# Kernel optimization log

Hardware: AMD Instinct MI355X
Metric: run time of the kernel (lower is better)

The kernel has to match this reference:

```python
import jax, jax.numpy as jnp
import numpy as np

K = 3
PAD = 1
EPS = 1e-5


def _unfold(x, k, pad):
    # torch.nn.Unfold(k, dilation=1, padding=pad, stride=1): output [B, C*k*k, L]
    # with channel-major ordering (c, ki, kj) in the second dim.
    B, C, H, W = x.shape
    xp = jnp.pad(x, ((0, 0), (0, 0), (pad, pad), (pad, pad)))
    Ho = H + 2 * pad - k + 1
    Wo = W + 2 * pad - k + 1
    patches = jnp.stack(
        [xp[:, :, i:i + Ho, j:j + Wo] for i in range(k) for j in range(k)],
        axis=2,
    )  # [B, C, k*k, Ho, Wo]
    return patches.reshape(B, C * k * k, Ho * Wo)


def _conv1x1(x, w, b):
    return jnp.einsum('bchw,oc->bohw', x, w) + b[None, :, None, None]


def _bn(x, g, b):
    # training-mode BatchNorm2d: batch stats over (B,H,W), biased variance
    mu = x.mean(axis=(0, 2, 3), keepdims=True)
    var = x.var(axis=(0, 2, 3), keepdims=True)
    return (x - mu) * jax.lax.rsqrt(var + EPS) * g[None, :, None, None] + b[None, :, None, None]


def _tri(x, w, b, g, be):
    return jax.nn.relu(_bn(_conv1x1(x, w, b), g, be))


def reference(x, w1, b1, g1, be1, w2, b2, g2, be2, wf, bf, gf, bef):
    B, C, H, W = x.shape
    k2 = K * K
    c = k2 // 2
    tri1 = _tri(x, w1, b1, g1, be1)  # key map  [B,C,H,W] (m=1)
    tri2 = _tri(x, w2, b2, g2, be2)  # query map
    # NOTE: faithful to source: plain row-major reshape of [B, C*k2, L] -> [B, C, L, k2]
    ku = _unfold(tri1, K, PAD).reshape(B, C, -1, k2)
    qu = _unfold(tri2, K, PAD).reshape(B, C, -1, k2)
    logits = ku * qu[..., c:c + 1] + ku[..., c:c + 1] * qu
    dl_weight = jax.nn.softmax(logits, axis=-1)[:, None]  # [B,1,C,L,k2]
    xu = _unfold(x, K, PAD).reshape(B, 1, C, -1, k2)       # m=1 -> [B,1,C,L,k2]
    # NOTE: faithful to source: row-major reshape to [B, C, k2, L], sum over axis -2
    pre = (dl_weight * xu).reshape(B, C, k2, -1).sum(axis=-2).reshape(B, C, H, W)
    return jax.nn.relu(_bn(_conv1x1(pre, wf, bf), gf, bef))


def setup_inputs() -> dict:
    key = jax.random.key(0)
    B, C, O, H, W = 4, 256, 256, 64, 64
    ks = jax.random.split(key, 4)
    s = 1.0 / np.sqrt(C)
    return {
        'x': jax.random.normal(ks[0], (B, C, H, W), dtype=jnp.float32),
        'w1': jax.random.normal(ks[1], (C, C), dtype=jnp.float32) * s,
        'b1': jnp.zeros((C,), jnp.float32),
        'g1': jnp.ones((C,), jnp.float32),
        'be1': jnp.zeros((C,), jnp.float32),
        'w2': jax.random.normal(ks[2], (C, C), dtype=jnp.float32) * s,
        'b2': jnp.zeros((C,), jnp.float32),
        'g2': jnp.ones((C,), jnp.float32),
        'be2': jnp.zeros((C,), jnp.float32),
        'wf': jax.random.normal(ks[3], (O, C), dtype=jnp.float32) * s,
        'bf': jnp.zeros((O,), jnp.float32),
        'gf': jnp.ones((O,), jnp.float32),
        'bef': jnp.zeros((O,), jnp.float32),
    }
```

## Files before the change

kernel.cpp:

```cpp
#include <hip/hip_runtime.h>
#include <hip/hip_bf16.h>

#define L 4096
#define CCH 256
#define NB 4
#define KP 40
#define GOF 72
#define LOG2E 1.4426950408889634f

typedef __attribute__((ext_vector_type(8))) short short8;
typedef __attribute__((ext_vector_type(4))) float f32x4;
typedef unsigned short ushort_t;

__device__ __forceinline__ unsigned short f2bf(float f) {
    unsigned u = __builtin_bit_cast(unsigned, f);
    u += 0x7FFF + ((u >> 16) & 1);
    return (unsigned short)(u >> 16);
}
__device__ __forceinline__ unsigned pk_bf16(float a, float b) {
    __hip_bfloat162 h = __float22bfloat162_rn(make_float2(a, b));
    unsigned u;
    __builtin_memcpy(&u, &h, 4);
    return u;
}
__device__ __forceinline__ float bflo(unsigned w) {
    return __builtin_bit_cast(float, w << 16);
}
__device__ __forceinline__ float bfhi(unsigned w) {
    return __builtin_bit_cast(float, w & 0xFFFF0000u);
}
__device__ __forceinline__ float bfu(ushort_t h) {
    return __builtin_bit_cast(float, (unsigned)h << 16);
}

__global__ __launch_bounds__(256) void wcvt_k(
    const float* __restrict__ w1, const float* __restrict__ w2,
    const float* __restrict__ wf,
    ushort_t* __restrict__ wb1, ushort_t* __restrict__ wb2,
    ushort_t* __restrict__ wbf)
{
    const int mb = blockIdx.x >> 6;
    const int i  = (blockIdx.x & 63) * 256 + threadIdx.x;
    const float* src = (mb == 0) ? w1 : (mb == 1) ? w2 : wf;
    ushort_t*    dst = (mb == 0) ? wb1 : (mb == 1) ? wb2 : wbf;
    float4 v = ((const float4*)src)[i];
    uint2 p;
    p.x = pk_bf16(v.x, v.y);
    p.y = pk_bf16(v.z, v.w);
    ((uint2*)dst)[i] = p;
}

__global__ __launch_bounds__(256, 2) void dual_gemm_k(
    const float* __restrict__ x,
    const ushort_t* __restrict__ wb1, const float* __restrict__ b1,
    const ushort_t* __restrict__ wb2, const float* __restrict__ b2,
    ushort_t* __restrict__ y1, ushort_t* __restrict__ y2)
{
    __shared__ short sA1[128 * KP];
    __shared__ short sA2[128 * KP];
    __shared__ short sB [64 * KP];

    const int tid = threadIdx.x;
    const int l0 = blockIdx.x * 64;
    const int o0 = blockIdx.y * 128;
    const int b  = blockIdx.z;

    const int wv = tid >> 6;
    const int lane = tid & 63;
    const int m = lane & 15;
    const int quad = lane >> 4;

    const float* xb = x + (size_t)b * CCH * L;

    const int sl = tid & 63, soct = tid >> 6;
    const int sr = tid & 127, sh = tid >> 7;

    f32x4 acc1[2][4], acc2[2][4];
    #pragma unroll
    for (int io = 0; io < 2; ++io)
        #pragma unroll
        for (int jl = 0; jl < 4; ++jl) {
            acc1[io][jl] = (f32x4){0.f,0.f,0.f,0.f};
            acc2[io][jl] = (f32x4){0.f,0.f,0.f,0.f};
        }

    for (int s = 0; s < 8; ++s) {
        const int k0 = s * 32;
        __syncthreads();
        {
            const float* xs = xb + (size_t)(k0 + soct * 8) * L + l0 + sl;
            float f[8];
            #pragma unroll
            for (int j = 0; j < 8; ++j) f[j] = xs[(size_t)j * L];
            uint4 v;
            v.x = pk_bf16(f[0], f[1]);
            v.y = pk_bf16(f[2], f[3]);
            v.z = pk_bf16(f[4], f[5]);
            v.w = pk_bf16(f[6], f[7]);
            *(uint4*)&sB[sl * KP + soct * 8] = v;
        }
        {
            const uint4* wp = (const uint4*)&wb1[(size_t)(o0 + sr) * CCH + k0 + sh * 16];
            uint4 p0 = wp[0], p1 = wp[1];
            *(uint4*)&sA1[sr * KP + sh * 16]     = p0;
            *(uint4*)&sA1[sr * KP + sh * 16 + 8] = p1;
            const uint4* wq = (const uint4*)&wb2[(size_t)(o0 + sr) * CCH + k0 + sh * 16];
            uint4 q0 = wq[0], q1 = wq[1];
            *(uint4*)&sA2[sr * KP + sh * 16]     = q0;
            *(uint4*)&sA2[sr * KP + sh * 16 + 8] = q1;
        }
        __syncthreads();
        short8 a1[2], a2[2], bf[4];
        #pragma unroll
        for (int io = 0; io < 2; ++io) {
            a1[io] = *(const short8*)&sA1[(wv * 32 + io * 16 + m) * KP + quad * 8];
            a2[io] = *(const short8*)&sA2[(wv * 32 + io * 16 + m) * KP + quad * 8];
        }
        #pragma unroll
        for (int jl = 0; jl < 4; ++jl)
            bf[jl] = *(const short8*)&sB[(jl * 16 + m) * KP + quad * 8];
        #pragma unroll
        for (int io = 0; io < 2; ++io)
            #pragma unroll
            for (int jl = 0; jl < 4; ++jl) {
                acc1[io][jl] = __builtin_amdgcn_mfma_f32_16x16x32_bf16(a1[io], bf[jl], acc1[io][jl], 0, 0, 0);
                acc2[io][jl] = __builtin_amdgcn_mfma_f32_16x16x32_bf16(a2[io], bf[jl], acc2[io][jl], 0, 0, 0);
            }
    }

    #pragma unroll
    for (int io = 0; io < 2; ++io)
        #pragma unroll
        for (int reg = 0; reg < 4; ++reg) {
            const int o = o0 + wv * 32 + io * 16 + quad * 4 + reg;
            const float bb1 = b1[o], bb2 = b2[o];
            const size_t ro = ((size_t)b * CCH + o) * L + l0 + m;
            unsigned u1a = pk_bf16(acc1[io][0][reg] + bb1, acc1[io][1][reg] + bb1);
            unsigned u1b = pk_bf16(acc1[io][2][reg] + bb1, acc1[io][3][reg] + bb1);
            unsigned u2a = pk_bf16(acc2[io][0][reg] + bb2, acc2[io][1][reg] + bb2);
            unsigned u2b = pk_bf16(acc2[io][2][reg] + bb2, acc2[io][3][reg] + bb2);
            y1[ro]      = (ushort_t)u1a;
            y1[ro + 16] = (ushort_t)(u1a >> 16);
            y1[ro + 32] = (ushort_t)u1b;
            y1[ro + 48] = (ushort_t)(u1b >> 16);
            y2[ro]      = (ushort_t)u2a;
            y2[ro + 16] = (ushort_t)(u2a >> 16);
            y2[ro + 32] = (ushort_t)u2b;
            y2[ro + 48] = (ushort_t)(u2b >> 16);
        }
}

__global__ __launch_bounds__(256, 2) void single_gemm_k(
    const ushort_t* __restrict__ x,
    const ushort_t* __restrict__ wb, const float* __restrict__ bb,
    ushort_t* __restrict__ y)
{
    __shared__ short sA[128 * KP];
    __shared__ short sB[64 * KP];

    const int tid = threadIdx.x;
    const int l0 = blockIdx.x * 64;
    const int o0 = blockIdx.y * 128;
    const int b  = blockIdx.z;

    const int wv = tid >> 6;
    const int lane = tid & 63;
    const int m = lane & 15;
    const int quad = lane >> 4;

    const ushort_t* xb = x + (size_t)b * CCH * L;

    const int sl = tid & 63, soct = tid >> 6;
    const int sr = tid & 127, sh = tid >> 7;

    f32x4 acc[2][4];
    #pragma unroll
    for (int io = 0; io < 2; ++io)
        #pragma unroll
        for (int jl = 0; jl < 4; ++jl)
            acc[io][jl] = (f32x4){0.f,0.f,0.f,0.f};

    for (int s = 0; s < 8; ++s) {
        const int k0 = s * 32;
        __syncthreads();
        {
            const ushort_t* xs = xb + (size_t)(k0 + soct * 8) * L + l0 + sl;
            short8 v;
            #pragma unroll
            for (int j = 0; j < 8; ++j) v[j] = (short)xs[(size_t)j * L];
            *(short8*)&sB[sl * KP + soct * 8] = v;
        }
        {
            const uint4* wp = (const uint4*)&wb[(size_t)(o0 + sr) * CCH + k0 + sh * 16];
            uint4 p0 = wp[0], p1 = wp[1];
            *(uint4*)&sA[sr * KP + sh * 16]     = p0;
            *(uint4*)&sA[sr * KP + sh * 16 + 8] = p1;
        }
        __syncthreads();
        short8 a[2], bf[4];
        #pragma unroll
        for (int io = 0; io < 2; ++io)
            a[io] = *(const short8*)&sA[(wv * 32 + io * 16 + m) * KP + quad * 8];
        #pragma unroll
        for (int jl = 0; jl < 4; ++jl)
            bf[jl] = *(const short8*)&sB[(jl * 16 + m) * KP + quad * 8];
        #pragma unroll
        for (int io = 0; io < 2; ++io)
            #pragma unroll
            for (int jl = 0; jl < 4; ++jl)
                acc[io][jl] = __builtin_amdgcn_mfma_f32_16x16x32_bf16(a[io], bf[jl], acc[io][jl], 0, 0, 0);
    }

    #pragma unroll
    for (int io = 0; io < 2; ++io)
        #pragma unroll
        for (int reg = 0; reg < 4; ++reg) {
            const int o = o0 + wv * 32 + io * 16 + quad * 4 + reg;
            const float b0 = bb[o];
            const size_t ro = ((size_t)b * CCH + o) * L + l0 + m;
            unsigned ua = pk_bf16(acc[io][0][reg] + b0, acc[io][1][reg] + b0);
            unsigned ub = pk_bf16(acc[io][2][reg] + b0, acc[io][3][reg] + b0);
            y[ro]      = (ushort_t)ua;
            y[ro + 16] = (ushort_t)(ua >> 16);
            y[ro + 32] = (ushort_t)ub;
            y[ro + 48] = (ushort_t)(ub >> 16);
        }
}

__device__ __forceinline__ void bn_stats_body(
    const ushort_t* y, const float* gamma, const float* beta,
    float* scale, float* shift, int c, int tid, float kscale)
{
    float s = 0.f, s2 = 0.f;
    for (int b = 0; b < NB; ++b) {
        const uint4* p = (const uint4*)(y + ((size_t)b * CCH + c) * L);
        #pragma unroll
        for (int r = 0; r < 2; ++r) {
            uint4 v = p[r * 256 + tid];
            unsigned w[4] = {v.x, v.y, v.z, v.w};
            #pragma unroll
            for (int u = 0; u < 4; ++u) {
                float a = bflo(w[u]), bb = bfhi(w[u]);
                s  += a + bb;
                s2 += a * a + bb * bb;
            }
        }
    }
    #pragma unroll
    for (int off = 32; off > 0; off >>= 1) {
        s  += __shfl_down(s, off);
        s2 += __shfl_down(s2, off);
    }
    __shared__ float red[2][4];
    if ((tid & 63) == 0) { red[0][tid >> 6] = s; red[1][tid >> 6] = s2; }
    __syncthreads();
    if (tid == 0) {
        float S  = red[0][0] + red[0][1] + red[0][2] + red[0][3];
        float S2 = red[1][0] + red[1][1] + red[1][2] + red[1][3];
        const float invN = 1.f / (NB * (float)L);
        float mean = S * invN;
        float var  = S2 * invN - mean * mean;
        float rstd = rsqrtf(var + 1e-5f);
        float g = gamma[c];
        scale[c] = kscale * g * rstd;
        shift[c] = kscale * (beta[c] - mean * g * rstd);
    }
}

__global__ __launch_bounds__(256) void bn_stats2_k(
    const ushort_t* __restrict__ y1, const float* __restrict__ g1, const float* __restrict__ be1,
    float* __restrict__ sc1, float* __restrict__ sh1,
    const ushort_t* __restrict__ y2, const float* __restrict__ g2, const float* __restrict__ be2,
    float* __restrict__ sc2, float* __restrict__ sh2)
{
    const int c = blockIdx.x & 255;
    if (blockIdx.x < 256) bn_stats_body(y1, g1, be1, sc1, sh1, c, threadIdx.x, LOG2E);
    else                  bn_stats_body(y2, g2, be2, sc2, sh2, c, threadIdx.x, 1.0f);
}

__global__ __launch_bounds__(512, 6) void attention_k(
    const float* __restrict__ x,
    const ushort_t* __restrict__ y1,
    const ushort_t* __restrict__ y2,
    const float* __restrict__ s1sc, const float* __restrict__ s1sh,
    const float* __restrict__ s2sc, const float* __restrict__ s2sh,
    ushort_t* __restrict__ pre)
{
    __shared__ unsigned sKQg[4240];
    __shared__ ushort_t sXg [4240];
    __shared__ float    accF[L];

    const int bc = blockIdx.x;
    const int tid = threadIdx.x;
    const int ch = bc & 255;
    const size_t off = (size_t)bc * L;

    const float sc1 = s1sc[ch], sh1 = s1sh[ch];
    const float sc2 = s2sc[ch], sh2 = s2sh[ch];

    if (tid < GOF)  { sKQg[tid] = 0; sXg[tid] = 0; }
    if (tid < 72)   { sKQg[GOF + 4096 + tid] = 0; sXg[GOF + 4096 + tid] = 0; }
    {
        float4 z = {0.f, 0.f, 0.f, 0.f};
        ((float4*)accF)[tid]       = z;
        ((float4*)accF)[tid + 512] = z;
    }
    {
        uint4 ak = ((const uint4*)(y1 + off))[tid];
        uint4 aq = ((const uint4*)(y2 + off))[tid];
        float4 xa = ((const float4*)(x + off))[2 * tid];
        float4 xb = ((const float4*)(x + off))[2 * tid + 1];
        unsigned wk[4] = {ak.x, ak.y, ak.z, ak.w};
        unsigned wq[4] = {aq.x, aq.y, aq.z, aq.w};
        unsigned kq[8];
        #pragma unroll
        for (int u = 0; u < 4; ++u) {
            float klo = fmaxf(fmaf(bflo(wk[u]), sc1, sh1), 0.f);
            float khi = fmaxf(fmaf(bfhi(wk[u]), sc1, sh1), 0.f);
            float qlo = fmaxf(fmaf(bflo(wq[u]), sc2, sh2), 0.f);
            float qhi = fmaxf(fmaf(bfhi(wq[u]), sc2, sh2), 0.f);
            kq[2*u]   = (unsigned)f2bf(klo) | ((unsigned)f2bf(qlo) << 16);
            kq[2*u+1] = (unsigned)f2bf(khi) | ((unsigned)f2bf(qhi) << 16);
        }
        *(uint4*)&sKQg[GOF + 8 * tid]     = make_uint4(kq[0], kq[1], kq[2], kq[3]);
        *(uint4*)&sKQg[GOF + 8 * tid + 4] = make_uint4(kq[4], kq[5], kq[6], kq[7]);
        float xv[8] = {xa.x, xa.y, xa.z, xa.w, xb.x, xb.y, xb.z, xb.w};
        unsigned xp[4];
        #pragma unroll
        for (int u = 0; u < 4; ++u)
            xp[u] = (unsigned)f2bf(xv[2*u]) | ((unsigned)f2bf(xv[2*u+1]) << 16);
        *(uint4*)&sXg[GOF + 8 * tid] = make_uint4(xp[0], xp[1], xp[2], xp[3]);
    }
    __syncthreads();

    {
        const int fbase = 9 * tid;
        #pragma unroll
        for (int r = 0; r < 8; ++r) {
            const int f  = fbase + 4608 * r;
            const int t  = f >> 12;
            const int fl = f & 4095;
            unsigned wv[9];
            float    xw[9];
            const bool fastp = (fl < 4088);
            if (fastp) {
                const int di = (t * 86) >> 8;
                const int dj = t - 3 * di;
                const int cbad = (dj == 0) ? 0 : ((dj == 2) ? 63 : 99);
                const int base = fl + (di << 6) + dj - 65 + GOF;
                #pragma unroll
                for (int j = 0; j < 9; ++j) {
                    wv[j] = sKQg[base + j];
                    xw[j] = bfu(sXg[base + j]);
                }
                #pragma unroll
                for (int j = 0; j < 9; ++j) {
                    int c = (fl + j) & 63;
                    bool bad = (c == cbad);
                    wv[j] = bad ? 0u  : wv[j];
                    xw[j] = bad ? 0.f : xw[j];
                }
            } else {
                #pragma unroll
                for (int j = 0; j < 9; ++j) {
                    int fj = f + j;
                    int tj = fj >> 12, lj = fj & 4095;
                    int dij = (tj * 86) >> 8, djj = tj - 3 * dij;
                    int idx = lj + (dij << 6) + djj - 65 + GOF;
                    unsigned wr = sKQg[idx];
                    float    xr = bfu(sXg[idx]);
                    int c = lj & 63;
                    int cb = (djj == 0) ? 0 : ((djj == 2) ? 63 : 99);
                    bool bad = (c == cb);
                    wv[j] = bad ? 0u  : wr;
                    xw[j] = bad ? 0.f : xr;
                }
            }
            const unsigned cw = wv[4];
            const float kc = bflo(cw), qc = bfhi(cw);
            float e[9];
            #pragma unroll
            for (int j = 0; j < 9; ++j)
                e[j] = __builtin_amdgcn_exp2f(bflo(wv[j]) * qc + kc * bfhi(wv[j]));
            float s = (((e[0] + e[1]) + (e[2] + e[3])) +
                       ((e[4] + e[5]) + (e[6] + e[7]))) + e[8];
            const float rinv = __builtin_amdgcn_rcpf(s);
            float cj[9];
            #pragma unroll
            for (int j = 0; j < 9; ++j)
                cj[j] = e[j] * rinv * xw[j];

            __syncthreads();
            if (tid < 455) {
                if (fastp) {
                    #pragma unroll
                    for (int j = 0; j < 9; ++j) accF[fl + j] += cj[j];
                } else {
                    #pragma unroll
                    for (int j = 0; j < 9; ++j) accF[(f + j) & 4095] += cj[j];
                }
            }
            __syncthreads();
            if (tid >= 455) {
                if (fastp) {
                    #pragma unroll
                    for (int j = 0; j < 9; ++j) accF[fl + j] += cj[j];
                } else {
                    #pragma unroll
                    for (int j = 0; j < 9; ++j) accF[(f + j) & 4095] += cj[j];
                }
            }
        }
    }
    __syncthreads();

    {
        unsigned* po = (unsigned*)(pre + off);
        #pragma unroll
        for (int rr = 0; rr < 4; ++rr) {
            const int p = rr * 512 + tid;
            po[p] = pk_bf16(accF[2 * p], accF[2 * p + 1]);
        }
    }
}

__global__ __launch_bounds__(256) void bn_fused_k(
    const ushort_t* __restrict__ yf,
    const float* __restrict__ gf, const float* __restrict__ bef,
    float* __restrict__ out)
{
    __shared__ uint4 sY[2048];
    __shared__ float red[2][4];
    __shared__ float fsc, fsh;

    const int c = blockIdx.x, tid = threadIdx.x;
    float s = 0.f, s2 = 0.f;
    #pragma unroll
    for (int b = 0; b < NB; ++b) {
        const uint4* p = (const uint4*)(yf + ((size_t)b * CCH + c) * L);
        #pragma unroll
        for (int r = 0; r < 2; ++r) {
            uint4 v = p[r * 256 + tid];
            sY[b * 512 + r * 256 + tid] = v;
            unsigned w[4] = {v.x, v.y, v.z, v.w};
            #pragma unroll
            for (int u = 0; u < 4; ++u) {
                float a = bflo(w[u]), bb = bfhi(w[u]);
                s  += a + bb;
                s2 += a * a + bb * bb;
            }
        }
    }
    #pragma unroll
    for (int off = 32; off > 0; off >>= 1) {
        s  += __shfl_down(s, off);
        s2 += __shfl_down(s2, off);
    }
    if ((tid & 63) == 0) { red[0][tid >> 6] = s; red[1][tid >> 6] = s2; }
    __syncthreads();
    if (tid == 0) {
        float S  = red[0][0] + red[0][1] + red[0][2] + red[0][3];
        float S2 = red[1][0] + red[1][1] + red[1][2] + red[1][3];
        const float invN = 1.f / (NB * (float)L);
        float mean = S * invN;
        float var  = S2 * invN - mean * mean;
        float rstd = rsqrtf(var + 1e-5f);
        float g = gf[c];
        fsc = g * rstd;
        fsh = bef[c] - mean * g * rstd;
    }
    __syncthreads();
    const float sc = fsc, sh = fsh;

    #pragma unroll
    for (int b = 0; b < NB; ++b) {
        float4* o = (float4*)(out + ((size_t)b * CCH + c) * L);
        #pragma unroll
        for (int r = 0; r < 2; ++r) {
            uint4 v = sY[b * 512 + r * 256 + tid];
            unsigned w[4] = {v.x, v.y, v.z, v.w};
            float4 o0, o1;
            o0.x = fmaxf(fmaf(bflo(w[0]), sc, sh), 0.f);
            o0.y = fmaxf(fmaf(bfhi(w[0]), sc, sh), 0.f);
            o0.z = fmaxf(fmaf(bflo(w[1]), sc, sh), 0.f);
            o0.w = fmaxf(fmaf(bfhi(w[1]), sc, sh), 0.f);
            o1.x = fmaxf(fmaf(bflo(w[2]), sc, sh), 0.f);
            o1.y = fmaxf(fmaf(bfhi(w[2]), sc, sh), 0.f);
            o1.z = fmaxf(fmaf(bflo(w[3]), sc, sh), 0.f);
            o1.w = fmaxf(fmaf(bfhi(w[3]), sc, sh), 0.f);
            int i = r * 256 + tid;
            o[2 * i]     = o0;
            o[2 * i + 1] = o1;
        }
    }
}

extern "C" void kernel_launch(void* const* d_in, const int* in_sizes, int n_in,
                              void* d_out, int out_size, void* d_ws, size_t ws_size,
                              hipStream_t stream) {
    const float* x   = (const float*)d_in[0];
    const float* w1  = (const float*)d_in[1];
    const float* b1  = (const float*)d_in[2];
    const float* g1  = (const float*)d_in[3];
    const float* be1 = (const float*)d_in[4];
    const float* w2  = (const float*)d_in[5];
    const float* b2  = (const float*)d_in[6];
    const float* g2  = (const float*)d_in[7];
    const float* be2 = (const float*)d_in[8];
    const float* wf  = (const float*)d_in[9];
    const float* bf  = (const float*)d_in[10];
    const float* gf  = (const float*)d_in[11];
    const float* bef = (const float*)d_in[12];
    float* out = (float*)d_out;

    const size_t NEL = (size_t)NB * CCH * L;
    ushort_t* y1b = (ushort_t*)d_ws;
    ushort_t* y2b = y1b + NEL;
    float* st = (float*)(y2b + NEL);
    float* s1sc = st,        *s1sh = st + 256;
    float* s2sc = st + 512,  *s2sh = st + 768;
    ushort_t* wb1 = (ushort_t*)(st + 1536);
    ushort_t* wb2 = wb1 + CCH * CCH;
    ushort_t* wbf = wb2 + CCH * CCH;

    wcvt_k<<<192, 256, 0, stream>>>(w1, w2, wf, wb1, wb2, wbf);
    dim3 gg(64, 2, 4);
    dual_gemm_k<<<gg, 256, 0, stream>>>(x, wb1, b1, wb2, b2, y1b, y2b);
    bn_stats2_k<<<512, 256, 0, stream>>>(y1b, g1, be1, s1sc, s1sh,
                                         y2b, g2, be2, s2sc, s2sh);
    attention_k<<<NB * CCH, 512, 0, stream>>>(x, y1b, y2b,
                                              s1sc, s1sh, s2sc, s2sh,
                                              y2b);
    single_gemm_k<<<gg, 256, 0, stream>>>(y2b, wbf, bf, y1b);
    bn_fused_k<<<256, 256, 0, stream>>>(y1b, gf, bef, out);
}
```

Before: 161.4 us.

## Double-buffer LDS tiles and prefetch next K-slice in both GEMM kernels

Both 1x1-conv GEMM kernels now keep two LDS buffers and load the next K-slice from global memory into registers while the current slice's MFMAs run, storing it to the other buffer afterwards. This removes one barrier per iteration and hides global-load latency behind compute. Launch-bounds occupancy hints are also raised (3 and 4 blocks per CU), which increases LDS use and register pressure and may force spills.

Measured after the change: 160.7 us. No clear change (-0.5%).

```diff
diff --git a/kernel.cpp b/kernel.cpp
--- a/kernel.cpp
+++ b/kernel.cpp
@@ -50,15 +50,15 @@
     ((uint2*)dst)[i] = p;
 }
 
-__global__ __launch_bounds__(256, 2) void dual_gemm_k(
+__global__ __launch_bounds__(256, 3) void dual_gemm_k(
     const float* __restrict__ x,
     const ushort_t* __restrict__ wb1, const float* __restrict__ b1,
     const ushort_t* __restrict__ wb2, const float* __restrict__ b2,
     ushort_t* __restrict__ y1, ushort_t* __restrict__ y2)
 {
-    __shared__ short sA1[128 * KP];
-    __shared__ short sA2[128 * KP];
-    __shared__ short sB [64 * KP];
+    __shared__ short sA1[2][128 * KP];
+    __shared__ short sA2[2][128 * KP];
+    __shared__ short sB [2][64 * KP];
 
     const int tid = threadIdx.x;
     const int l0 = blockIdx.x * 64;
@@ -84,48 +84,59 @@
             acc2[io][jl] = (f32x4){0.f,0.f,0.f,0.f};
         }
 
+    float fx[8];
+    uint4 pw1a, pw1b, pw2a, pw2b;
+
+    auto LOADT = [&](int s) {
+        const int k0 = s * 32;
+        const float* xs = xb + (size_t)(k0 + soct * 8) * L + l0 + sl;
+        #pragma unroll
+        for (int j = 0; j < 8; ++j) fx[j] = xs[(size_t)j * L];
+        const uint4* wp = (const uint4*)&wb1[(size_t)(o0 + sr) * CCH + k0 + sh * 16];
+        pw1a = wp[0]; pw1b = wp[1];
+        const uint4* wq = (const uint4*)&wb2[(size_t)(o0 + sr) * CCH + k0 + sh * 16];
+        pw2a = wq[0]; pw2b = wq[1];
+    };
+    auto STORET = [&](int buf) {
+        uint4 v;
+        v.x = pk_bf16(fx[0], fx[1]);
+        v.y = pk_bf16(fx[2], fx[3]);
+        v.z = pk_bf16(fx[4], fx[5]);
+        v.w = pk_bf16(fx[6], fx[7]);
+        *(uint4*)&sB[buf][sl * KP + soct * 8] = v;
+        *(uint4*)&sA1[buf][sr * KP + sh * 16]     = pw1a;
+        *(uint4*)&sA1[buf][sr * KP + sh * 16 + 8] = pw1b;
+        *(uint4*)&sA2[buf][sr * KP + sh * 16]     = pw2a;
+        *(uint4*)&sA2[buf][sr * KP + sh * 16 + 8] = pw2b;
+    };
+
+    LOADT(0);
+    STORET(0);
+    __syncthreads();
+
     for (int s = 0; s < 8; ++s) {
-        const int k0 = s * 32;
-        __syncthreads();
-        {
-            const float* xs = xb + (size_t)(k0 + soct * 8) * L + l0 + sl;
-            float f[8];
-            #pragma unroll
-            for (int j = 0; j < 8; ++j) f[j] = xs[(size_t)j * L];
-            uint4 v;
-            v.x = pk_bf16(f[0], f[1]);
-            v.y = pk_bf16(f[2], f[3]);
-            v.z = pk_bf16(f[4], f[5]);
-            v.w = pk_bf16(f[6], f[7]);
-            *(uint4*)&sB[sl * KP + soct * 8] = v;
-        }
-        {
-            const uint4* wp = (const uint4*)&wb1[(size_t)(o0 + sr) * CCH + k0 + sh * 16];
-            uint4 p0 = wp[0], p1 = wp[1];
-            *(uint4*)&sA1[sr * KP + sh * 16]     = p0;
-            *(uint4*)&sA1[sr * KP + sh * 16 + 8] = p1;
-            const uint4* wq = (const uint4*)&wb2[(size_t)(o0 + sr) * CCH + k0 + sh * 16];
-            uint4 q0 = wq[0], q1 = wq[1];
-            *(uint4*)&sA2[sr * KP + sh * 16]     = q0;
-            *(uint4*)&sA2[sr * KP + sh * 16 + 8] = q1;
-        }
-        __syncthreads();
-        short8 a1[2], a2[2], bf[4];
+        const int buf = s & 1;
+        if (s < 7) LOADT(s + 1);
+
+        short8 a1[2], a2[2], bfr[4];
         #pragma unroll
         for (int io = 0; io < 2; ++io) {
-            a1[io] = *(const short8*)&sA1[(wv * 32 + io * 16 + m) * KP + quad * 8];
-            a2[io] = *(const short8*)&sA2[(wv * 32 + io * 16 + m) * KP + quad * 8];
+            a1[io] = *(const short8*)&sA1[buf][(wv * 32 + io * 16 + m) * KP + quad * 8];
+            a2[io] = *(const short8*)&sA2[buf][(wv * 32 + io * 16 + m) * KP + quad * 8];
         }
         #pragma unroll
         for (int jl = 0; jl < 4; ++jl)
-            bf[jl] = *(const short8*)&sB[(jl * 16 + m) * KP + quad * 8];
+            bfr[jl] = *(const short8*)&sB[buf][(jl * 16 + m) * KP + quad * 8];
         #pragma unroll
         for (int io = 0; io < 2; ++io)
             #pragma unroll
             for (int jl = 0; jl < 4; ++jl) {
-                acc1[io][jl] = __builtin_amdgcn_mfma_f32_16x16x32_bf16(a1[io], bf[jl], acc1[io][jl], 0, 0, 0);
-                acc2[io][jl] = __builtin_amdgcn_mfma_f32_16x16x32_bf16(a2[io], bf[jl], acc2[io][jl], 0, 0, 0);
+                acc1[io][jl] = __builtin_amdgcn_mfma_f32_16x16x32_bf16(a1[io], bfr[jl], acc1[io][jl], 0, 0, 0);
+                acc2[io][jl] = __builtin_amdgcn_mfma_f32_16x16x32_bf16(a2[io], bfr[jl], acc2[io][jl], 0, 0, 0);
             }
+
+        if (s < 7) STORET(buf ^ 1);
+        __syncthreads();
     }
 
     #pragma unroll
@@ -150,13 +161,13 @@
         }
 }
 
-__global__ __launch_bounds__(256, 2) void single_gemm_k(
+__global__ __launch_bounds__(256, 4) void single_gemm_k(
     const ushort_t* __restrict__ x,
     const ushort_t* __restrict__ wb, const float* __restrict__ bb,
     ushort_t* __restrict__ y)
 {
-    __shared__ short sA[128 * KP];
-    __shared__ short sB[64 * KP];
+    __shared__ short sA[2][128 * KP];
+    __shared__ short sB[2][64 * KP];
 
     const int tid = threadIdx.x;
     const int l0 = blockIdx.x * 64;
@@ -180,35 +191,49 @@
         for (int jl = 0; jl < 4; ++jl)
             acc[io][jl] = (f32x4){0.f,0.f,0.f,0.f};
 
+    ushort_t hx[8];
+    uint4 pwa, pwb;
+
+    auto LOADT = [&](int s) {
+        const int k0 = s * 32;
+        const ushort_t* xs = xb + (size_t)(k0 + soct * 8) * L + l0 + sl;
+        #pragma unroll
+        for (int j = 0; j < 8; ++j) hx[j] = xs[(size_t)j * L];
+        const uint4* wp = (const uint4*)&wb[(size_t)(o0 + sr) * CCH + k0 + sh * 16];
+        pwa = wp[0]; pwb = wp[1];
+    };
+    auto STORET = [&](int buf) {
+        short8 v;
+        #pragma unroll
+        for (int j = 0; j < 8; ++j) v[j] = (short)hx[j];
+        *(short8*)&sB[buf][sl * KP + soct * 8] = v;
+        *(uint4*)&sA[buf][sr * KP + sh * 16]     = pwa;
+        *(uint4*)&sA[buf][sr * KP + sh * 16 + 8] = pwb;
+    };
+
+    LOADT(0);
+    STORET(0);
+    __syncthreads();
+
     for (int s = 0; s < 8; ++s) {
-        const int k0 = s * 32;
-        __syncthreads();
-        {
-            const ushort_t* xs = xb + (size_t)(k0 + soct * 8) * L + l0 + sl;
-            short8 v;
-            #pragma unroll
-            for (int j = 0; j < 8; ++j) v[j] = (short)xs[(size_t)j * L];
-            *(short8*)&sB[sl * KP + soct * 8] = v;
-        }
-        {
-            const uint4* wp = (const uint4*)&wb[(size_t)(o0 + sr) * CCH + k0 + sh * 16];
-            uint4 p0 = wp[0], p1 = wp[1];
-            *(uint4*)&sA[sr * KP + sh * 16]     = p0;
-            *(uint4*)&sA[sr * KP + sh * 16 + 8] = p1;
-        }
-        __syncthreads();
-        short8 a[2], bf[4];
+        const int buf = s & 1;
+        if (s < 7) LOADT(s + 1);
+
+        short8 a[2], bfr[4];
         #pragma unroll
         for (int io = 0; io < 2; ++io)
-            a[io] = *(const short8*)&sA[(wv * 32 + io * 16 + m) * KP + quad * 8];
+            a[io] = *(const short8*)&sA[buf][(wv * 32 + io * 16 + m) * KP + quad * 8];
         #pragma unroll
         for (int jl = 0; jl < 4; ++jl)
-            bf[jl] = *(const short8*)&sB[(jl * 16 + m) * KP + quad * 8];
+            bfr[jl] = *(const short8*)&sB[buf][(jl * 16 + m) * KP + quad * 8];
         #pragma unroll
         for (int io = 0; io < 2; ++io)
             #pragma unroll
             for (int jl = 0; jl < 4; ++jl)
-                acc[io][jl] = __builtin_amdgcn_mfma_f32_16x16x32_bf16(a[io], bf[jl], acc[io][jl], 0, 0, 0);
+                acc[io][jl] = __builtin_amdgcn_mfma_f32_16x16x32_bf16(a[io], bfr[jl], acc[io][jl], 0, 0, 0);
+
+        if (s < 7) STORET(buf ^ 1);
+        __syncthreads();
     }
 
     #pragma unroll
```
